# Kernel optimization log

Measured on AMD Instinct MI355X. Metric: run time of the kernel, lower is better.

Reference implementation:

```python
import jax, jax.numpy as jnp
import numpy as np
from jax import lax

B, W, K = 64, 128, 64      # batch, window_size, n_features
KS = 7                      # conv kernel size
EF = W                      # feature-attn embed dim (defaults to window_size, GATv1)
ET = 2 * K                  # temporal-attn embed dim (n_features doubled by GATv2)
H = 256                     # GRU hidden
FH = 256                    # forecast MLP hidden
ALPHA = 0.2                 # leaky relu slope


def _leaky(v):
    return jnp.where(v >= 0, v, ALPHA * v)


def setup_inputs() -> dict:
    key = jax.random.key(0)
    ks = jax.random.split(key, 20)
    s = 0.05
    inp = {
        "x": jax.random.normal(ks[0], (B, W, K), jnp.float32),
        # ConvLayer
        "conv_w": jax.random.normal(ks[1], (K, K, KS), jnp.float32) * s,
        "conv_b": jnp.zeros((K,), jnp.float32),
        # FeatureAttentionLayer (GATv1): lin W->EF, a:[2EF,1], bias [K,K]
        "feat_lin_w": jax.random.normal(ks[2], (EF, W), jnp.float32) * s,
        "feat_lin_b": jnp.zeros((EF,), jnp.float32),
        "feat_a": jax.random.normal(ks[3], (2 * EF, 1), jnp.float32) * s,
        "feat_bias": jnp.zeros((K, K), jnp.float32),
        # TemporalAttentionLayer (GATv2): lin 2K->ET, a:[ET,1], bias [W,W]
        "temp_lin_w": jax.random.normal(ks[4], (ET, 2 * K), jnp.float32) * s,
        "temp_lin_b": jnp.zeros((ET,), jnp.float32),
        "temp_a": jax.random.normal(ks[5], (ET, 1), jnp.float32) * s,
        "temp_bias": jnp.zeros((W, W), jnp.float32),
        # GRU (1 layer), input dim 3K
        "gru_wih": jax.random.normal(ks[6], (3 * H, 3 * K), jnp.float32) * s,
        "gru_whh": jax.random.normal(ks[7], (3 * H, H), jnp.float32) * s,
        "gru_bih": jnp.zeros((3 * H,), jnp.float32),
        "gru_bhh": jnp.zeros((3 * H,), jnp.float32),
        "fc0_w": jax.random.normal(ks[8], (FH, H), jnp.float32) * s,
        "fc0_b": jnp.zeros((FH,), jnp.float32),
        "fc1_w": jax.random.normal(ks[9], (FH, FH), jnp.float32) * s,
        "fc1_b": jnp.zeros((FH,), jnp.float32),
        "fc2_w": jax.random.normal(ks[10], (FH, FH), jnp.float32) * s,
        "fc2_b": jnp.zeros((FH,), jnp.float32),
        "fc3_w": jax.random.normal(ks[11], (K, FH), jnp.float32) * s,
        "fc3_b": jnp.zeros((K,), jnp.float32),
    }
    return inp


def _forward(x, conv_w, conv_b, feat_lin_w, feat_lin_b, feat_a, feat_bias,
             temp_lin_w, temp_lin_b, temp_a, temp_bias,
             gru_wih, gru_whh, gru_bih, gru_bhh,
             fc0_w, fc0_b, fc1_w, fc1_b, fc2_w, fc2_b, fc3_w, fc3_b):
    # --- ConvLayer: pad (k-1)//2 both sides, Conv1d K->K, ReLU ---
    pad = (KS - 1) // 2
    xc = x.transpose(0, 2, 1)                                   # [B,K,W]
    xc = jnp.pad(xc, ((0, 0), (0, 0), (pad, pad)))
    y = lax.conv_general_dilated(xc, conv_w, (1,), 'VALID',
                                 dimension_numbers=('NCH', 'OIH', 'NCH'))
    y = jax.nn.relu(y + conv_b[None, :, None]).transpose(0, 2, 1)  # [B,W,K]

    # --- FeatureAttentionLayer (GATv1): e_ij = leaky((Wx_i||Wx_j)·a) ---
    xf = y.transpose(0, 2, 1)                                   # [B,K,W]
    Wx = xf @ feat_lin_w.T + feat_lin_b                         # [B,K,EF]
    s1 = Wx @ feat_a[:EF, 0]                                    # [B,K]
    s2 = Wx @ feat_a[EF:, 0]                                    # [B,K]
    e_f = _leaky(s1[:, :, None] + s2[:, None, :]) + feat_bias   # [B,K,K]
    att_f = jax.nn.softmax(e_f, axis=2)
    h_feat = jax.nn.sigmoid(att_f @ xf).transpose(0, 2, 1)      # [B,W,K]

    # --- TemporalAttentionLayer (GATv2): g = leaky(lin(x_i||x_j)); e = g·a ---
    W1, W2 = temp_lin_w[:, :K], temp_lin_w[:, K:]               # split lin over concat halves
    p = y @ W1.T                                                # [B,W,ET]
    q = y @ W2.T                                                # [B,W,ET]
    g = _leaky(p[:, :, None, :] + q[:, None, :, :] + temp_lin_b)  # [B,W,W,ET]
    e_t = (g @ temp_a)[..., 0] + temp_bias                      # [B,W,W]
    att_t = jax.nn.softmax(e_t, axis=2)
    h_temp = jax.nn.sigmoid(att_t @ y)                          # [B,W,K]

    # --- concat + GRU over time ---
    z = jnp.concatenate([y, h_feat, h_temp], axis=2)            # [B,W,3K]

    def gru_step(h, xt):
        gi = xt @ gru_wih.T + gru_bih                           # [B,3H]
        gh = h @ gru_whh.T + gru_bhh
        ir, iz, inn = jnp.split(gi, 3, axis=1)
        hr, hz, hn = jnp.split(gh, 3, axis=1)
        r = jax.nn.sigmoid(ir + hr)
        zg = jax.nn.sigmoid(iz + hz)
        n = jnp.tanh(inn + r * hn)
        return (1.0 - zg) * n + zg * h, None

    h0 = jnp.zeros((z.shape[0], H), z.dtype)
    h_end, _ = lax.scan(gru_step, h0, z.transpose(1, 0, 2))     # [B,H]

    # --- Forecasting MLP (eval mode: dropout is identity) ---
    v = jax.nn.relu(h_end @ fc0_w.T + fc0_b)
    v = jax.nn.relu(v @ fc1_w.T + fc1_b)
    v = jax.nn.relu(v @ fc2_w.T + fc2_b)
    return v @ fc3_w.T + fc3_b                                  # [B,K]


def reference(x, conv_w, conv_b, feat_lin_w, feat_lin_b, feat_a, feat_bias,
              temp_lin_w, temp_lin_b, temp_a, temp_bias,
              gru_wih, gru_whh, gru_bih, gru_bhh,
              fc0_w, fc0_b, fc1_w, fc1_b, fc2_w, fc2_b, fc3_w, fc3_b):
    return _forward(x, conv_w, conv_b, feat_lin_w, feat_lin_b, feat_a, feat_bias,
                    temp_lin_w, temp_lin_b, temp_a, temp_bias,
                    gru_wih, gru_whh, gru_bih, gru_bhh,
                    fc0_w, fc0_b, fc1_w, fc1_b, fc2_w, fc2_b, fc3_w, fc3_b)
```

## Files before the change

### kernel.cpp

```cpp
#include <hip/hip_runtime.h>
#include <hip/hip_bf16.h>

typedef unsigned int uint;
typedef _Float16 half2_t __attribute__((ext_vector_type(2)));

union H2U { uint u; half2_t h; };

#if defined(__has_builtin)
#if __has_builtin(__builtin_amdgcn_fdot2)
#define HAVE_FDOT2 1
#endif
#endif

__device__ __forceinline__ float dot2acc(uint w, uint hh, float acc) {
    H2U a; a.u = w; H2U b; b.u = hh;
#ifdef HAVE_FDOT2
    return __builtin_amdgcn_fdot2(a.h, b.h, acc, false);
#else
    return acc + (float)a.h.x * (float)b.h.x + (float)a.h.y * (float)b.h.y;
#endif
}

#define OFF_Y    0u
#define OFF_Z    524288u
#define OFF_GI   2097152u
#define OFF_WHH  8388608u
#define OFF_C12  8486912u
#define OFF_DD   8487168u
#define OFF_HEND 8487424u

__global__ __launch_bounds__(256) void k_pack_prep(const float* __restrict__ whh, uint* __restrict__ w16,
                                                   const float* __restrict__ flw, const float* __restrict__ flb,
                                                   const float* __restrict__ fa, float* __restrict__ c12,
                                                   float* __restrict__ dd) {
    __shared__ float red[256];
    int bx = blockIdx.x, tid = threadIdx.x;
    if (bx < 384) {
        int idx = bx * 256 + tid;
        int tidq = idx / 192;
        int rem = idx - tidq * 192;
        int rp = rem >> 6;
        int i = rem & 63;
        int half = tidq >> 8;
        int mloc = tidq & 255;
        int row = 3 * mloc + rp;
        int pc = half * 64 + i;
        float a = whh[(size_t)row * 256 + 2 * pc];
        float b = whh[(size_t)row * 256 + 2 * pc + 1];
        H2U u; u.h.x = (_Float16)a; u.h.y = (_Float16)b;
        w16[idx] = u.u;
    } else {
        if (tid < 128) {
            float a = 0.f, b = 0.f;
            for (int e = 0; e < 128; ++e) {
                float w = flw[e * 128 + tid];
                a = fmaf(w, fa[e], a);
                b = fmaf(w, fa[128 + e], b);
            }
            c12[tid] = a;
            c12[128 + tid] = b;
        }
        int e = tid & 127;
        red[tid] = (tid < 128) ? flb[e] * fa[e] : flb[e] * fa[128 + e];
        __syncthreads();
        if (tid < 2) {
            float s = 0.f;
            for (int q = 0; q < 128; ++q) s += red[tid * 128 + q];
            dd[tid] = s;
        }
    }
}

__global__ __launch_bounds__(256) void k_conv(const float* __restrict__ x, const float* __restrict__ cw,
                                              const float* __restrict__ cb, float* __restrict__ y,
                                              float* __restrict__ z) {
    __shared__ float xT[64][41];
    __shared__ float cwL[64 * 64 * 7];
    int b = blockIdx.y, w0 = blockIdx.x * 32, tid = threadIdx.x;
    for (int idx = tid; idx < 38 * 64; idx += 256) {
        int wl = idx / 64, k = idx % 64;
        int wg = w0 - 3 + wl;
        xT[k][wl] = (wg >= 0 && wg < 128) ? x[((size_t)b * 128 + wg) * 64 + k] : 0.f;
    }
    for (int idx = tid; idx < 64 * 64 * 7; idx += 256) cwL[idx] = cw[idx];
    __syncthreads();
    int w_l = tid % 32, kog = tid / 32;
    float acc[8];
#pragma unroll
    for (int i = 0; i < 8; ++i) acc[i] = 0.f;
    for (int ki = 0; ki < 64; ++ki) {
        float x7[7];
#pragma unroll
        for (int u = 0; u < 7; ++u) x7[u] = xT[ki][w_l + u];
#pragma unroll
        for (int koi = 0; koi < 8; ++koi) {
            const float* wp = &cwL[((kog * 8 + koi) * 64 + ki) * 7];
#pragma unroll
            for (int u = 0; u < 7; ++u) acc[koi] = fmaf(x7[u], wp[u], acc[koi]);
        }
    }
    int w = w0 + w_l;
#pragma unroll
    for (int koi = 0; koi < 8; ++koi) {
        int ko = kog * 8 + koi;
        float v = acc[koi] + cb[ko];
        v = v > 0.f ? v : 0.f;
        y[((size_t)b * 128 + w) * 64 + ko] = v;
        z[((size_t)b * 128 + w) * 192 + ko] = v;
    }
}

__global__ __launch_bounds__(256) void k_feat(const float* __restrict__ y, const float* __restrict__ c12,
                                              const float* __restrict__ dd, const float* __restrict__ fb,
                                              float* __restrict__ z) {
    int b = blockIdx.y, w0 = blockIdx.x * 32, tid = threadIdx.x;
    __shared__ float s1L[64], s2L[64];
    __shared__ float attL[64][65];
    __shared__ float yL[32][64];
    __shared__ float cL[256];
    cL[tid] = c12[tid];
    for (int idx = tid; idx < 32 * 64; idx += 256) {
        int wl = idx / 64, j = idx % 64;
        yL[wl][j] = y[((size_t)b * 128 + w0 + wl) * 64 + j];
    }
    __syncthreads();
    if (tid < 128) {
        int k = tid % 64;
        const float* c = (tid < 64) ? cL : cL + 128;
        float acc = 0.f;
        for (int w = 0; w < 128; ++w) acc = fmaf(y[((size_t)b * 128 + w) * 64 + k], c[w], acc);
        if (tid < 64) s1L[k] = acc + dd[0]; else s2L[k] = acc + dd[1];
    }
    __syncthreads();
    if (tid < 64) {
        int k = tid;
        float s1 = s1L[k];
        float m = -1e30f;
        for (int j = 0; j < 64; ++j) {
            float v = s1 + s2L[j];
            float l = fmaxf(v, 0.2f * v);
            float e = l + fb[k * 64 + j];
            attL[k][j] = e;
            m = fmaxf(m, e);
        }
        float s = 0.f;
        for (int j = 0; j < 64; ++j) { float e = __expf(attL[k][j] - m); attL[k][j] = e; s += e; }
        float inv = 1.f / s;
        for (int j = 0; j < 64; ++j) attL[k][j] *= inv;
    }
    __syncthreads();
    int k_l = tid % 64, wg = tid / 64;
    for (int wi = 0; wi < 8; ++wi) {
        int wl = wg * 8 + wi;
        float acc = 0.f;
#pragma unroll 16
        for (int j = 0; j < 64; ++j) acc = fmaf(attL[k_l][j], yL[wl][j], acc);
        float hv = 1.f / (1.f + __expf(-acc));
        z[((size_t)b * 128 + w0 + wl) * 192 + 64 + k_l] = hv;
    }
}

__global__ __launch_bounds__(512) void k_temp(const float* __restrict__ y, const float* __restrict__ tlw,
                                              const float* __restrict__ tlb, const float* __restrict__ ta,
                                              const float* __restrict__ tbias, float* __restrict__ z) {
    int b = blockIdx.y, i0 = blockIdx.x * 32, tid = threadIdx.x;
    __shared__ __align__(16) float yT[64][132];
    __shared__ __align__(16) float qL[128][128];
    __shared__ __align__(16) float pL[32][128];
    __shared__ __align__(16) float etL[32][128];
    __shared__ __align__(16) float taL[128];
    __shared__ float mred[32][8], sred[32][8];
    __shared__ float mrow[32], invL[32];
    if (tid < 128) taL[tid] = ta[tid];
    for (int idx = tid; idx < 8192; idx += 512) {
        int j = idx >> 6, k = idx & 63;
        yT[k][j] = y[((size_t)b * 128 + j) * 64 + k];
    }
    __syncthreads();
    {
        int c = tid & 127, ih = tid >> 7;
        float w1r[64];
        const float4* w1p = (const float4*)(tlw + c * 128);
#pragma unroll
        for (int q4 = 0; q4 < 16; ++q4) {
            float4 v = w1p[q4];
            w1r[4 * q4] = v.x; w1r[4 * q4 + 1] = v.y; w1r[4 * q4 + 2] = v.z; w1r[4 * q4 + 3] = v.w;
        }
        float base = tlb[c];
#pragma unroll
        for (int ilb = 0; ilb < 2; ++ilb) {
            int j0 = i0 + ih * 8 + ilb * 4;
            float4 acc = {base, base, base, base};
            for (int k = 0; k < 64; ++k) {
                float4 yv = *((const float4*)&yT[k][j0]);
                float w = w1r[k];
                acc.x = fmaf(yv.x, w, acc.x); acc.y = fmaf(yv.y, w, acc.y);
                acc.z = fmaf(yv.z, w, acc.z); acc.w = fmaf(yv.w, w, acc.w);
            }
            int il = ih * 8 + ilb * 4;
            pL[il][c] = acc.x; pL[il + 1][c] = acc.y; pL[il + 2][c] = acc.z; pL[il + 3][c] = acc.w;
        }
    }
    {
        int j = tid & 127, ch = tid >> 7;
        float yreg[64];
#pragma unroll
        for (int k = 0; k < 64; ++k) yreg[k] = yT[k][j];
        for (int cc = 0; cc < 32; ++cc) {
            int c = __builtin_amdgcn_readfirstlane(ch * 32 + cc);
            const float* w2 = tlw + c * 128 + 64;
            float acc = 0.f;
#pragma unroll
            for (int k = 0; k < 64; ++k) acc = fmaf(yreg[k], w2[k], acc);
            qL[c][j] = acc;
        }
    }
    __syncthreads();
    {
        int jg = tid & 31, ih = tid >> 5;
        int j0 = jg * 4;
        int il0 = ih * 2;
        float4 acc0 = *((const float4*)(tbias + (size_t)(i0 + il0) * 128 + j0));
        float4 acc1 = *((const float4*)(tbias + (size_t)(i0 + il0 + 1) * 128 + j0));
        for (int c0 = 0; c0 < 128; c0 += 4) {
            float4 ta4 = *((const float4*)&taL[c0]);
            float4 p0 = *((const float4*)&pL[il0][c0]);
            float4 p1 = *((const float4*)&pL[il0 + 1][c0]);
            float4 q0 = *((const float4*)&qL[c0 + 0][j0]);
            float4 q1 = *((const float4*)&qL[c0 + 1][j0]);
            float4 q2 = *((const float4*)&qL[c0 + 2][j0]);
            float4 q3 = *((const float4*)&qL[c0 + 3][j0]);
#define ETSTEP(qv, tac, pa, pb) { \
            float u; \
            u = (pa) + qv.x; acc0.x = fmaf(fmaxf(u, 0.2f * u), (tac), acc0.x); \
            u = (pa) + qv.y; acc0.y = fmaf(fmaxf(u, 0.2f * u), (tac), acc0.y); \
            u = (pa) + qv.z; acc0.z = fmaf(fmaxf(u, 0.2f * u), (tac), acc0.z); \
            u = (pa) + qv.w; acc0.w = fmaf(fmaxf(u, 0.2f * u), (tac), acc0.w); \
            u = (pb) + qv.x; acc1.x = fmaf(fmaxf(u, 0.2f * u), (tac), acc1.x); \
            u = (pb) + qv.y; acc1.y = fmaf(fmaxf(u, 0.2f * u), (tac), acc1.y); \
            u = (pb) + qv.z; acc1.z = fmaf(fmaxf(u, 0.2f * u), (tac), acc1.z); \
            u = (pb) + qv.w; acc1.w = fmaf(fmaxf(u, 0.2f * u), (tac), acc1.w); }
            ETSTEP(q0, ta4.x, p0.x, p1.x)
            ETSTEP(q1, ta4.y, p0.y, p1.y)
            ETSTEP(q2, ta4.z, p0.z, p1.z)
            ETSTEP(q3, ta4.w, p0.w, p1.w)
#undef ETSTEP
        }
        *((float4*)&etL[il0][j0]) = acc0;
        *((float4*)&etL[il0 + 1][j0]) = acc1;
    }
    __syncthreads();
    if (tid < 256) {
        int il = tid >> 3, seg = tid & 7;
        const float4* ep = (const float4*)&etL[il][seg * 16];
        float m = -1e30f;
#pragma unroll
        for (int q = 0; q < 4; ++q) {
            float4 e = ep[q];
            m = fmaxf(m, fmaxf(fmaxf(e.x, e.y), fmaxf(e.z, e.w)));
        }
        mred[il][seg] = m;
    }
    __syncthreads();
    if (tid < 32) {
        float m = mred[tid][0];
#pragma unroll
        for (int s = 1; s < 8; ++s) m = fmaxf(m, mred[tid][s]);
        mrow[tid] = m;
    }
    __syncthreads();
    if (tid < 256) {
        int il = tid >> 3, seg = tid & 7;
        float m = mrow[il];
        float4* ep = (float4*)&etL[il][seg * 16];
        float s = 0.f;
#pragma unroll
        for (int q = 0; q < 4; ++q) {
            float4 e = ep[q];
            e.x = __expf(e.x - m); e.y = __expf(e.y - m);
            e.z = __expf(e.z - m); e.w = __expf(e.w - m);
            s += (e.x + e.y) + (e.z + e.w);
            ep[q] = e;
        }
        sred[il][seg] = s;
    }
    __syncthreads();
    if (tid < 32) {
        float s = 0.f;
#pragma unroll
        for (int q = 0; q < 8; ++q) s += sred[tid][q];
        invL[tid] = 1.f / s;
    }
    __syncthreads();
    {
        int k = tid & 63, ig = tid >> 6;
        float acc[4] = {0.f, 0.f, 0.f, 0.f};
        const float* yb = y + (size_t)b * 128 * 64 + k;
        for (int j0 = 0; j0 < 128; j0 += 4) {
            float yv[4];
#pragma unroll
            for (int jj = 0; jj < 4; ++jj) yv[jj] = yb[(size_t)(j0 + jj) * 64];
#pragma unroll
            for (int ii = 0; ii < 4; ++ii) {
                int il = ig * 4 + ii;
                float4 ev = *((const float4*)&etL[il][j0]);
                acc[ii] = fmaf(ev.x, yv[0], acc[ii]);
                acc[ii] = fmaf(ev.y, yv[1], acc[ii]);
                acc[ii] = fmaf(ev.z, yv[2], acc[ii]);
                acc[ii] = fmaf(ev.w, yv[3], acc[ii]);
            }
        }
#pragma unroll
        for (int ii = 0; ii < 4; ++ii) {
            int il = ig * 4 + ii;
            float hv = 1.f / (1.f + __expf(-acc[ii] * invL[il]));
            z[((size_t)b * 128 + i0 + il) * 192 + 128 + k] = hv;
        }
    }
}

__global__ __launch_bounds__(256) void k_gi(const float* __restrict__ z, const float* __restrict__ wih,
                                            const float* __restrict__ bih, float* __restrict__ gi) {
    int o0 = blockIdx.x * 128;
    int bt0 = blockIdx.y * 64;
    int tid = threadIdx.x;
    __shared__ __align__(16) float zL[64][68];
    __shared__ float wL[128][65];
    int ol = tid & 31;
    int r8 = (tid >> 5) * 8;
    float acc[8][4];
#pragma unroll
    for (int rr = 0; rr < 8; ++rr)
#pragma unroll
        for (int oo = 0; oo < 4; ++oo) acc[rr][oo] = 0.f;
    for (int mc = 0; mc < 3; ++mc) {
        int m0 = mc * 64;
        __syncthreads();
        {
            int mq = (tid & 15) * 4;
            int r = tid >> 4;
#pragma unroll
            for (int it = 0; it < 4; ++it, r += 16) {
                float4 v = *((const float4*)&z[(size_t)(bt0 + r) * 192 + m0 + mq]);
                *((float4*)&zL[r][mq]) = v;
            }
            int o = tid >> 4;
#pragma unroll
            for (int it = 0; it < 8; ++it, o += 16) {
                float4 v = *((const float4*)&wih[(size_t)(o0 + o) * 192 + m0 + mq]);
                wL[o][mq] = v.x; wL[o][mq + 1] = v.y; wL[o][mq + 2] = v.z; wL[o][mq + 3] = v.w;
            }
        }
        __syncthreads();
        for (int mb = 0; mb < 64; mb += 4) {
            float4 zv[8];
#pragma unroll
            for (int rr = 0; rr < 8; ++rr) zv[rr] = *((const float4*)&zL[r8 + rr][mb]);
#pragma unroll
            for (int mi = 0; mi < 4; ++mi) {
                float wv[4];
#pragma unroll
                for (int oo = 0; oo < 4; ++oo) wv[oo] = wL[ol + 32 * oo][mb + mi];
#pragma unroll
                for (int rr = 0; rr < 8; ++rr) {
                    float zc = (mi == 0) ? zv[rr].x : (mi == 1) ? zv[rr].y : (mi == 2) ? zv[rr].z : zv[rr].w;
#pragma unroll
                    for (int oo = 0; oo < 4; ++oo) acc[rr][oo] = fmaf(zc, wv[oo], acc[rr][oo]);
                }
            }
        }
    }
    float bo[4];
#pragma unroll
    for (int oo = 0; oo < 4; ++oo) bo[oo] = bih[o0 + ol + 32 * oo];
#pragma unroll
    for (int rr = 0; rr < 8; ++rr)
#pragma unroll
        for (int oo = 0; oo < 4; ++oo)
            gi[(size_t)(bt0 + r8 + rr) * 768 + o0 + ol + 32 * oo] = acc[rr][oo] + bo[oo];
}

#define KEEP4(W) asm volatile("" : "+v"(W.x), "+v"(W.y), "+v"(W.z), "+v"(W.w))
__global__ __launch_bounds__(512)
__attribute__((amdgpu_waves_per_eu(2, 2)))
void k_gru(const float* __restrict__ gi,
           const uint* __restrict__ w16,
           const float* __restrict__ bhh,
           float* __restrict__ hend) {
    int b = blockIdx.x, tid = threadIdx.x;
    int half = tid >> 8, mloc = tid & 255;
    int t = tid & 255;
    __shared__ __align__(16) uint4 hp4s[32];
    __shared__ float sH[2][768];
    uint4 wv[48];
    {
        const uint4* wp = (const uint4*)(w16 + (size_t)tid * 192);
#pragma unroll
        for (int i = 0; i < 48; ++i) wv[i] = wp[i];
    }
    float br = 0.f, bz = 0.f, bn = 0.f;
    if (tid < 256) { br = bhh[t]; bz = bhh[256 + t]; bn = bhh[512 + t]; }
    float h = 0.f;
    if (tid < 32) { uint4 zz; zz.x = zz.y = zz.z = zz.w = 0u; hp4s[tid] = zz; }
    __syncthreads();
    const float* gib = gi + (size_t)b * 128 * 768;
    const uint4* hbase = hp4s + half * 16;
    int m3 = 3 * mloc;
    for (int s = 0; s < 128; ++s) {
#pragma unroll
        for (int i = 0; i < 48; ++i) KEEP4(wv[i]);
        float gr = 0.f, gz = 0.f, gn = 0.f;
        if (tid < 256) {
            gr = gib[s * 768 + t];
            gz = gib[s * 768 + 256 + t];
            gn = gib[s * 768 + 512 + t];
        }
        float a0 = 0.f, a1 = 0.f, b0 = 0.f, b1 = 0.f, c0 = 0.f, c1 = 0.f;
#pragma unroll
        for (int j = 0; j < 16; ++j) {
            uint4 hv = hbase[j];
            uint4 wa = wv[j];
            uint4 wb = wv[16 + j];
            uint4 wc = wv[32 + j];
            a0 = dot2acc(wa.x, hv.x, a0); a1 = dot2acc(wa.y, hv.y, a1);
            a0 = dot2acc(wa.z, hv.z, a0); a1 = dot2acc(wa.w, hv.w, a1);
            b0 = dot2acc(wb.x, hv.x, b0); b1 = dot2acc(wb.y, hv.y, b1);
            b0 = dot2acc(wb.z, hv.z, b0); b1 = dot2acc(wb.w, hv.w, b1);
            c0 = dot2acc(wc.x, hv.x, c0); c1 = dot2acc(wc.y, hv.y, c1);
            c0 = dot2acc(wc.z, hv.z, c0); c1 = dot2acc(wc.w, hv.w, c1);
        }
        sH[half][m3 + 0] = a0 + a1;
        sH[half][m3 + 1] = b0 + b1;
        sH[half][m3 + 2] = c0 + c1;
        __syncthreads();
        if (tid < 256) {
            float hr = sH[0][t] + sH[1][t] + br;
            float hz = sH[0][256 + t] + sH[1][256 + t] + bz;
            float hn = sH[0][512 + t] + sH[1][512 + t] + bn;
            float r  = 1.f / (1.f + __expf(-(gr + hr)));
            float zg = 1.f / (1.f + __expf(-(gz + hz)));
            float nx = gn + r * hn;
            float n  = 1.f - 2.f / (1.f + __expf(2.f * nx));
            h = (1.f - zg) * n + zg * h;
            ((_Float16*)hp4s)[t] = (_Float16)h;
        }
        __syncthreads();
    }
    if (tid < 256) hend[b * 256 + t] = h;
}

__global__ __launch_bounds__(256) void k_fc(const float* __restrict__ hend,
                                            const float* __restrict__ w0, const float* __restrict__ b0,
                                            const float* __restrict__ w1, const float* __restrict__ b1,
                                            const float* __restrict__ w2, const float* __restrict__ b2,
                                            const float* __restrict__ w3, const float* __restrict__ b3,
                                            float* __restrict__ out) {
    int b = blockIdx.x, tid = threadIdx.x;
    __shared__ float bufA[256], bufB[256];
    bufA[tid] = hend[b * 256 + tid];
    __syncthreads();
    {
        float acc = b0[tid];
        const float* wrow = &w0[tid * 256];
#pragma unroll 8
        for (int m = 0; m < 256; ++m) acc = fmaf(wrow[m], bufA[m], acc);
        bufB[tid] = fmaxf(acc, 0.f);
    }
    __syncthreads();
    {
        float acc = b1[tid];
        const float* wrow = &w1[tid * 256];
#pragma unroll 8
        for (int m = 0; m < 256; ++m) acc = fmaf(wrow[m], bufB[m], acc);
        bufA[tid] = fmaxf(acc, 0.f);
    }
    __syncthreads();
    {
        float acc = b2[tid];
        const float* wrow = &w2[tid * 256];
#pragma unroll 8
        for (int m = 0; m < 256; ++m) acc = fmaf(wrow[m], bufA[m], acc);
        bufB[tid] = fmaxf(acc, 0.f);
    }
    __syncthreads();
    if (tid < 64) {
        float acc = b3[tid];
        const float* wrow = &w3[tid * 256];
#pragma unroll 8
        for (int m = 0; m < 256; ++m) acc = fmaf(wrow[m], bufB[m], acc);
        out[b * 64 + tid] = acc;
    }
}

extern "C" void kernel_launch(void* const* d_in, const int* in_sizes, int n_in,
                              void* d_out, int out_size, void* d_ws, size_t ws_size,
                              hipStream_t stream) {
    const float* x    = (const float*)d_in[0];
    const float* cw   = (const float*)d_in[1];
    const float* cb   = (const float*)d_in[2];
    const float* flw  = (const float*)d_in[3];
    const float* flb  = (const float*)d_in[4];
    const float* fa   = (const float*)d_in[5];
    const float* fb   = (const float*)d_in[6];
    const float* tlw  = (const float*)d_in[7];
    const float* tlb  = (const float*)d_in[8];
    const float* ta   = (const float*)d_in[9];
    const float* tb   = (const float*)d_in[10];
    const float* wih  = (const float*)d_in[11];
    const float* whh  = (const float*)d_in[12];
    const float* bih  = (const float*)d_in[13];
    const float* bhh  = (const float*)d_in[14];
    const float* fc0w = (const float*)d_in[15];
    const float* fc0b = (const float*)d_in[16];
    const float* fc1w = (const float*)d_in[17];
    const float* fc1b = (const float*)d_in[18];
    const float* fc2w = (const float*)d_in[19];
    const float* fc2b = (const float*)d_in[20];
    const float* fc3w = (const float*)d_in[21];
    const float* fc3b = (const float*)d_in[22];

    float* wsf  = (float*)d_ws;
    float* y    = wsf + OFF_Y;
    float* z    = wsf + OFF_Z;
    float* gi   = wsf + OFF_GI;
    uint*  w16  = (uint*)(wsf + OFF_WHH);
    float* c12  = wsf + OFF_C12;
    float* dd   = wsf + OFF_DD;
    float* hend = wsf + OFF_HEND;
    float* out  = (float*)d_out;

    k_pack_prep<<<385, 256, 0, stream>>>(whh, w16, flw, flb, fa, c12, dd);
    k_conv<<<dim3(4, 64), 256, 0, stream>>>(x, cw, cb, y, z);
    k_feat<<<dim3(4, 64), 256, 0, stream>>>(y, c12, dd, fb, z);
    k_temp<<<dim3(4, 64), 512, 0, stream>>>(y, tlw, tlb, ta, tb, z);
    k_gi<<<dim3(6, 128), 256, 0, stream>>>(z, wih, bih, gi);
    k_gru<<<64, 512, 0, stream>>>(gi, w16, bhh, hend);
    k_fc<<<64, 256, 0, stream>>>(hend, fc0w, fc0b, fc1w, fc1b, fc2w, fc2b, fc3w, fc3b, out);
}
```

Before: 416.3 us.

## Compute GRU recurrent matvec with MFMA 16x16x32 f16 instead of fdot2

Result: faster. 400.1 us (-3.9%).

```diff
diff --git a/kernel.cpp b/kernel.cpp
--- a/kernel.cpp
+++ b/kernel.cpp
@@ -3,23 +3,11 @@
 
 typedef unsigned int uint;
 typedef _Float16 half2_t __attribute__((ext_vector_type(2)));
+typedef _Float16 half8 __attribute__((ext_vector_type(8)));
+typedef float f32x4 __attribute__((ext_vector_type(4)));
 
 union H2U { uint u; half2_t h; };
-
-#if defined(__has_builtin)
-#if __has_builtin(__builtin_amdgcn_fdot2)
-#define HAVE_FDOT2 1
-#endif
-#endif
-
-__device__ __forceinline__ float dot2acc(uint w, uint hh, float acc) {
-    H2U a; a.u = w; H2U b; b.u = hh;
-#ifdef HAVE_FDOT2
-    return __builtin_amdgcn_fdot2(a.h, b.h, acc, false);
-#else
-    return acc + (float)a.h.x * (float)b.h.x + (float)a.h.y * (float)b.h.y;
-#endif
-}
+union U4H8 { uint4 u; half8 h; };
 
 #define OFF_Y    0u
 #define OFF_Z    524288u
@@ -38,17 +26,18 @@
     if (bx < 384) {
         int idx = bx * 256 + tid;
         int tidq = idx / 192;
-        int rem = idx - tidq * 192;
-        int rp = rem >> 6;
-        int i = rem & 63;
-        int half = tidq >> 8;
-        int mloc = tidq & 255;
-        int row = 3 * mloc + rp;
-        int pc = half * 64 + i;
-        float a = whh[(size_t)row * 256 + 2 * pc];
-        float b = whh[(size_t)row * 256 + 2 * pc + 1];
-        H2U u; u.h.x = (_Float16)a; u.h.y = (_Float16)b;
-        w16[idx] = u.u;
+        int r = idx - tidq * 192;
+        int u = r >> 5;
+        int q = (r >> 2) & 7;
+        int p = r & 3;
+        int w = tidq >> 6;
+        int l = tidq & 63;
+        int row = w * 96 + u * 16 + (l & 15);
+        int colb = q * 32 + (l >> 4) * 8 + 2 * p;
+        float a = whh[(size_t)row * 256 + colb];
+        float b = whh[(size_t)row * 256 + colb + 1];
+        H2U uu; uu.h.x = (_Float16)a; uu.h.y = (_Float16)b;
+        w16[idx] = uu.u;
     } else {
         if (tid < 128) {
             float a = 0.f, b = 0.f;
@@ -380,7 +369,6 @@
             gi[(size_t)(bt0 + r8 + rr) * 768 + o0 + ol + 32 * oo] = acc[rr][oo] + bo[oo];
 }
 
-#define KEEP4(W) asm volatile("" : "+v"(W.x), "+v"(W.y), "+v"(W.z), "+v"(W.w))
 __global__ __launch_bounds__(512)
 __attribute__((amdgpu_waves_per_eu(2, 2)))
 void k_gru(const float* __restrict__ gi,
@@ -388,61 +376,62 @@
            const float* __restrict__ bhh,
            float* __restrict__ hend) {
     int b = blockIdx.x, tid = threadIdx.x;
-    int half = tid >> 8, mloc = tid & 255;
+    int w = tid >> 6, l = tid & 63;
     int t = tid & 255;
-    __shared__ __align__(16) uint4 hp4s[32];
-    __shared__ float sH[2][768];
-    uint4 wv[48];
-    {
-        const uint4* wp = (const uint4*)(w16 + (size_t)tid * 192);
-#pragma unroll
-        for (int i = 0; i < 48; ++i) wv[i] = wp[i];
+    int quad = l >> 4;
+    __shared__ __align__(16) _Float16 hp16[256];
+    __shared__ float sH[768];
+    half8 bfr[48];
+    {
+        const uint4* wp4 = (const uint4*)(w16 + (size_t)tid * 192);
+#pragma unroll
+        for (int i = 0; i < 48; ++i) { U4H8 c_; c_.u = wp4[i]; bfr[i] = c_.h; }
     }
     float br = 0.f, bz = 0.f, bn = 0.f;
     if (tid < 256) { br = bhh[t]; bz = bhh[256 + t]; bn = bhh[512 + t]; }
     float h = 0.f;
-    if (tid < 32) { uint4 zz; zz.x = zz.y = zz.z = zz.w = 0u; hp4s[tid] = zz; }
+    if (tid < 128) ((uint*)hp16)[tid] = 0u;
     __syncthreads();
     const float* gib = gi + (size_t)b * 128 * 768;
-    const uint4* hbase = hp4s + half * 16;
-    int m3 = 3 * mloc;
+    const uint4* hp4 = (const uint4*)hp16;
     for (int s = 0; s < 128; ++s) {
-#pragma unroll
-        for (int i = 0; i < 48; ++i) KEEP4(wv[i]);
         float gr = 0.f, gz = 0.f, gn = 0.f;
         if (tid < 256) {
             gr = gib[s * 768 + t];
             gz = gib[s * 768 + 256 + t];
             gn = gib[s * 768 + 512 + t];
         }
-        float a0 = 0.f, a1 = 0.f, b0 = 0.f, b1 = 0.f, c0 = 0.f, c1 = 0.f;
-#pragma unroll
-        for (int j = 0; j < 16; ++j) {
-            uint4 hv = hbase[j];
-            uint4 wa = wv[j];
-            uint4 wb = wv[16 + j];
-            uint4 wc = wv[32 + j];
-            a0 = dot2acc(wa.x, hv.x, a0); a1 = dot2acc(wa.y, hv.y, a1);
-            a0 = dot2acc(wa.z, hv.z, a0); a1 = dot2acc(wa.w, hv.w, a1);
-            b0 = dot2acc(wb.x, hv.x, b0); b1 = dot2acc(wb.y, hv.y, b1);
-            b0 = dot2acc(wb.z, hv.z, b0); b1 = dot2acc(wb.w, hv.w, b1);
-            c0 = dot2acc(wc.x, hv.x, c0); c1 = dot2acc(wc.y, hv.y, c1);
-            c0 = dot2acc(wc.z, hv.z, c0); c1 = dot2acc(wc.w, hv.w, c1);
-        }
-        sH[half][m3 + 0] = a0 + a1;
-        sH[half][m3 + 1] = b0 + b1;
-        sH[half][m3 + 2] = c0 + c1;
+        f32x4 acc[6];
+#pragma unroll
+        for (int u = 0; u < 6; ++u) acc[u] = (f32x4){0.f, 0.f, 0.f, 0.f};
+#pragma unroll
+        for (int q = 0; q < 8; ++q) {
+            U4H8 c_; c_.u = hp4[q * 4 + quad];
+            half8 av = c_.h;
+#pragma unroll
+            for (int u = 0; u < 6; ++u)
+                acc[u] = __builtin_amdgcn_mfma_f32_16x16x32_f16(av, bfr[u * 8 + q], acc[u], 0, 0, 0);
+        }
+        if (l < 16) {
+            int base = w * 96 + l;
+            sH[base +  0] = acc[0][0];
+            sH[base + 16] = acc[1][0];
+            sH[base + 32] = acc[2][0];
+            sH[base + 48] = acc[3][0];
+            sH[base + 64] = acc[4][0];
+            sH[base + 80] = acc[5][0];
+        }
         __syncthreads();
         if (tid < 256) {
-            float hr = sH[0][t] + sH[1][t] + br;
-            float hz = sH[0][256 + t] + sH[1][256 + t] + bz;
-            float hn = sH[0][512 + t] + sH[1][512 + t] + bn;
+            float hr = sH[t] + br;
+            float hz = sH[256 + t] + bz;
+            float hn = sH[512 + t] + bn;
             float r  = 1.f / (1.f + __expf(-(gr + hr)));
             float zg = 1.f / (1.f + __expf(-(gz + hz)));
             float nx = gn + r * hn;
             float n  = 1.f - 2.f / (1.f + __expf(2.f * nx));
             h = (1.f - zg) * n + zg * h;
-            ((_Float16*)hp4s)[t] = (_Float16)h;
+            hp16[t] = (_Float16)h;
         }
         __syncthreads();
     }
```
